# Optimization experiments

Measured on AMD Instinct MI355X. Metric: run time of the kernel, lower is better.

Reference implementation:

```python
import jax, jax.numpy as jnp
from jax import lax
import numpy as np

B, T, L = 8, 24, 145
DHID, DFRAME, DEMB, DGCN, V = 1024, 2500, 128, 512, 1024
PF = 300
DINP = DHID + DFRAME + DEMB + DGCN   # 4164 = LSTM input size
DCONT = DHID + DINP                  # 5188 = cont_t size
FLAT = 64 * 7 * 7                    # 3136
BN_EPS = 1e-5
BN_INV = float(1.0 / np.sqrt(1.0 + BN_EPS))  # eval BN with running mean 0, var 1


def setup_inputs() -> dict:
    key = jax.random.key(0)
    ks = iter(jax.random.split(key, 48))
    rn = lambda *s: jax.random.normal(next(ks), s, jnp.float32)
    w = lambda *s: 0.02 * rn(*s)
    return dict(
        enc=rn(B, L, DHID),
        frames=rn(B, T, 512, 7, 7),
        gcn_embedding=rn(B, DGCN),
        h0=jnp.zeros((B, DHID), jnp.float32),
        c0=jnp.zeros((B, DHID), jnp.float32),
        conv1_w=w(256, 512), conv1_b=jnp.zeros((256,), jnp.float32),
        bn1_g=jnp.ones((256,), jnp.float32), bn1_b=jnp.zeros((256,), jnp.float32),
        conv2_w=w(64, 256), conv2_b=jnp.zeros((64,), jnp.float32),
        bn2_g=jnp.ones((64,), jnp.float32), bn2_b=jnp.zeros((64,), jnp.float32),
        fc_w=w(DFRAME, FLAT), fc_b=jnp.zeros((DFRAME,), jnp.float32),
        hfc_w=w(DHID, DHID), hfc_b=jnp.zeros((DHID,), jnp.float32),
        w_ih=w(4 * DHID, DINP), w_hh=w(4 * DHID, DHID),
        b_ih=jnp.zeros((4 * DHID,), jnp.float32), b_hh=jnp.zeros((4 * DHID,), jnp.float32),
        go=0.1 * rn(DEMB),
        emb_w=w(V, DEMB),
        actor_w=w(DEMB, DCONT), actor_b=jnp.zeros((DEMB,), jnp.float32),
        d1_w=w(FLAT, DCONT), d1_b=jnp.zeros((FLAT,), jnp.float32),
        dconv3_w=w(64, 32, 4, 4), dconv3_b=jnp.zeros((32,), jnp.float32),
        bnm2_g=jnp.ones((32,), jnp.float32), bnm2_b=jnp.zeros((32,), jnp.float32),
        dconv2_w=w(32, 16, 4, 4), dconv2_b=jnp.zeros((16,), jnp.float32),
        bnm1_g=jnp.ones((16,), jnp.float32), bnm1_b=jnp.zeros((16,), jnp.float32),
        dconv1_w=w(16, 1, 4, 4), dconv1_b=jnp.zeros((1,), jnp.float32),
    )


def _bn_eval(x, g, b):
    # BatchNorm2d in eval mode with running_mean=0, running_var=1
    return g[None, :, None, None] * (x * BN_INV) + b[None, :, None, None]


def _up2(x):
    # UpsamplingNearest2d(scale_factor=2)
    return jnp.repeat(jnp.repeat(x, 2, axis=2), 2, axis=3)


def _deconv(x, w, b):
    # ConvTranspose2d(k=4, s=2, p=1); torch weight layout (in, out, kH, kW)
    k = jnp.flip(w, (2, 3)).transpose(1, 0, 2, 3)  # -> (out, in, kH, kW)
    y = lax.conv_general_dilated(x, k, window_strides=(1, 1), padding=((2, 2), (2, 2)),
                                 lhs_dilation=(2, 2),
                                 dimension_numbers=('NCHW', 'OIHW', 'NCHW'))
    return y + b[None, :, None, None]


def reference(enc, frames, gcn_embedding, h0, c0,
              conv1_w, conv1_b, bn1_g, bn1_b, conv2_w, conv2_b, bn2_g, bn2_b, fc_w, fc_b,
              hfc_w, hfc_b, w_ih, w_hh, b_ih, b_hh, go, emb_w, actor_w, actor_b,
              d1_w, d1_b, dconv3_w, dconv3_b, bnm2_g, bnm2_b,
              dconv2_w, dconv2_b, bnm1_g, bnm1_b, dconv1_w, dconv1_b):

    def vis_encode(frame):  # [B,512,7,7] -> [B,DFRAME]
        x = jnp.einsum('bchw,oc->bohw', frame, conv1_w) + conv1_b[None, :, None, None]
        x = jax.nn.relu(_bn_eval(x, bn1_g, bn1_b))
        x = jnp.einsum('bchw,oc->bohw', x, conv2_w) + conv2_b[None, :, None, None]
        x = jax.nn.relu(_bn_eval(x, bn2_g, bn2_b))
        return x.reshape(-1, FLAT) @ fc_w.T + fc_b

    def mask_decode(cont):  # [B,DCONT] -> [B,1,300,300]
        x = jax.nn.relu(cont @ d1_w.T + d1_b).reshape(-1, 64, 7, 7)
        x = _deconv(_up2(x), dconv3_w, dconv3_b)          # 14 -> 28
        x = jax.nn.relu(_bn_eval(x, bnm2_g, bnm2_b))
        x = _deconv(_up2(x), dconv2_w, dconv2_b)          # 56 -> 112
        x = jax.nn.relu(_bn_eval(x, bnm1_g, bnm1_b))
        x = _deconv(x, dconv1_w, dconv1_b)                # 112 -> 224
        return jax.image.resize(x, (x.shape[0], 1, PF, PF), method='bilinear')

    def step(carry, frame_t):
        h, c, e_t = carry
        vis = vis_encode(frame_t)
        hq = h @ hfc_w.T + hfc_b
        score = jax.nn.softmax(jnp.einsum('bld,bd->bl', enc, hq), axis=1)  # [B,L]
        weighted = jnp.einsum('bl,bld->bd', score, enc)
        inp = jnp.concatenate([vis, weighted, e_t, gcn_embedding], axis=1)  # [B,DINP]
        gates = inp @ w_ih.T + b_ih + h @ w_hh.T + b_hh
        i, f, g, o = jnp.split(gates, 4, axis=1)
        c_new = jax.nn.sigmoid(f) * c + jax.nn.sigmoid(i) * jnp.tanh(g)
        h_new = jax.nn.sigmoid(o) * jnp.tanh(c_new)
        cont = jnp.concatenate([h_new, inp], axis=1)  # [B,DCONT]
        action = (cont @ actor_w.T + actor_b) @ emb_w.T  # [B,V]
        mask = mask_decode(cont)
        e_new = emb_w[jnp.argmax(action, axis=1)]  # greedy feed-back
        return (h_new, c_new, e_new), (action, mask, score[:, :, None])

    e0 = jnp.tile(go[None, :], (enc.shape[0], 1))
    (h_T, c_T, _), (actions, masks, attns) = lax.scan(
        step, (h0, c0, e0), jnp.swapaxes(frames, 0, 1))
    out_action = jnp.swapaxes(actions, 0, 1)   # [B,T,V]
    out_mask = jnp.swapaxes(masks, 0, 1)       # [B,T,1,300,300]
    out_attn = jnp.swapaxes(attns, 0, 1)       # [B,T,L,1]
    return (out_action, out_mask, out_attn, h_T, c_T)
```

## Files before the change

### kernel.cpp

```cpp
#include <hip/hip_runtime.h>
#include <cstdint>
#include <cstddef>

#define DEV __device__ __forceinline__
typedef short bf16x8 __attribute__((ext_vector_type(8)));
typedef float fl4 __attribute__((ext_vector_type(4)));
typedef float f32x4 __attribute__((ext_vector_type(4)));
typedef unsigned short u16;

#define BN_INV 0.9999950000375f

DEV float b2f(u16 u){ return __uint_as_float(((unsigned)u)<<16); }
DEV u16 f2b(float f){ unsigned u = __float_as_uint(f); unsigned r = (u + 0x7FFFu + ((u>>16)&1u))>>16; return (u16)r; }

DEV bf16x8 load8(const u16* p){ return *(const bf16x8*)p; }
DEV bf16x8 load8(const float* p){
  fl4 a = *(const fl4*)p; fl4 b = *(const fl4*)(p+4);
  bf16x8 r;
  r[0]=(short)f2b(a[0]); r[1]=(short)f2b(a[1]); r[2]=(short)f2b(a[2]); r[3]=(short)f2b(a[3]);
  r[4]=(short)f2b(b[0]); r[5]=(short)f2b(b[1]); r[6]=(short)f2b(b[2]); r[7]=(short)f2b(b[3]);
  return r;
}


__global__ __launch_bounds__(256) void k_pack_frames(const float* __restrict__ fr, u16* __restrict__ XT){
  int bt = blockIdx.x, tid = threadIdx.x;
  for (int e=0;e<128;e++){
    int flat = e*256 + tid;
    int p = flat>>9, c = flat&511;
    u16 v = 0;
    if (p < 49) v = f2b(fr[((size_t)bt*512 + c)*49 + p]);
    XT[((size_t)bt*64 + p)*512 + c] = v;
  }
}

__global__ __launch_bounds__(256) void k_pack_wseq(const float* __restrict__ w_ih, const float* __restrict__ w_hh,
                                                   u16* __restrict__ wseq){
  int r = blockIdx.x, tid = threadIdx.x;
  const float* wr = w_ih + (size_t)r*4164;
  for (int j=tid;j<2176;j+=256){
    float v = (j < 1024) ? w_hh[(size_t)r*1024 + j] : wr[2500 + (j-1024)];
    wseq[(size_t)r*2176 + j] = f2b(v);
  }
}

__global__ __launch_bounds__(256) void k_pack_dseq(const float* __restrict__ d1_w, const float* __restrict__ actor_w,
                                                   u16* __restrict__ dseq){
  int r = blockIdx.x, tid = threadIdx.x;
  const float* wr = (r < 3136) ? (d1_w + (size_t)r*5188) : (actor_w + (size_t)(r-3136)*5188);
  for (int j=tid;j<2176;j+=256){
    float v = (j < 1024) ? wr[j] : wr[3524 + (j-1024)];
    dseq[(size_t)r*2176 + j] = f2b(v);
  }
}

__global__ __launch_bounds__(256) void k_pack_wvg(const float* __restrict__ w_ih, u16* __restrict__ wvg, int rbase){
  int r = rbase + blockIdx.x, tid = threadIdx.x;
  const float* wr = w_ih + (size_t)r*4164;
  u16* dst = wvg + (size_t)blockIdx.x*3072;
  for (int j=tid;j<3072;j+=256){
    float v = 0.f;
    if (j < 2500) v = wr[j];
    else if (j < 3012) v = wr[3652 + (j-2500)];
    dst[j] = f2b(v);
  }
}

__global__ __launch_bounds__(256) void k_pack_dvg(const float* __restrict__ d1_w, const float* __restrict__ actor_w,
                                                  u16* __restrict__ dvg, int rbase){
  int r = rbase + blockIdx.x, tid = threadIdx.x;
  const float* wr = (r < 3136) ? (d1_w + (size_t)r*5188) : (actor_w + (size_t)(r-3136)*5188);
  u16* dst = dvg + (size_t)blockIdx.x*3072;
  for (int j=tid;j<3072;j+=256){
    float v = 0.f;
    if (j < 2500) v = wr[1024 + j];
    else if (j < 3012) v = wr[4676 + (j-2500)];
    dst[j] = f2b(v);
  }
}

__global__ __launch_bounds__(256) void k_hfcT(const float* __restrict__ hfc_w, u16* __restrict__ hfcT){
  int idx = blockIdx.x*256 + threadIdx.x;
  int k = idx>>10, o = idx&1023;
  hfcT[idx] = f2b(hfc_w[o*1024 + k]);
}

DEV u16 wt_map(const float* w, int n, int k, int CIN, int COUT){
  int o = n % COUT; int cls = n / COUT;
  if (cls >= 4) return 0;
  int py = cls>>1, px = cls&1;
  int i = k/9; int dd = k - i*9; int dy = dd/3, dx = dd - dy*3;
  if (i >= CIN) return 0;
  int ky = (py==0) ? (dy==0 ? 3 : (dy==1 ? 1 : -1)) : (dy==1 ? 2 : (dy==2 ? 0 : -1));
  int kx = (px==0) ? (dx==0 ? 3 : (dx==1 ? 1 : -1)) : (dx==1 ? 2 : (dx==2 ? 0 : -1));
  if (ky < 0 || kx < 0) return 0;
  return f2b(w[((i*COUT + o)*4 + ky)*4 + kx]);
}

__global__ __launch_bounds__(256) void k_misc(
  const float* b_ih, const float* b_hh, const float* d1_b, const float* actor_b,
  const float* emb_w, const float* h0, const float* c0,
  const float* dw3, const float* dw2, const float* dw1,
  float* bias_g, float* bias_da, u16* embT, float* hb0, float* cws,
  u16* Wt3, u16* Wt2, u16* Wt1)
{
  int blk = blockIdx.x, tid = threadIdx.x;
  if (blk < 16){ int i = blk*256+tid; if (i<4096) bias_g[i] = b_ih[i] + b_hh[i]; }
  else if (blk < 29){ int i = (blk-16)*256+tid; if (i<3264) bias_da[i] = (i<3136)? d1_b[i] : actor_b[i-3136]; }
  else if (blk < 541){ int i = (blk-29)*256+tid; int j = i>>10, v = i&1023; embT[i] = f2b(emb_w[v*128 + j]); }
  else if (blk < 573){ int i = (blk-541)*256+tid; if (i<8192){ hb0[i] = h0[i]; cws[i] = c0[i]; } }
  else if (blk < 574){ for (int i=tid;i<2560;i+=256){ int n=i/160, k=i-n*160; Wt1[i] = wt_map(dw1,n,k,16,1); } }
  else if (blk < 590){ for (int i=(blk-574)*256+tid; i<18432; i+=16*256){ int n=i/288, k=i-n*288; Wt2[i] = wt_map(dw2,n,k,32,16); } }
  else { for (int i=(blk-590)*256+tid; i<73728; i+=168*256){ int n=i/576, k=i-n*576; Wt3[i] = wt_map(dw3,n,k,64,32); } }
}

__global__ __launch_bounds__(256) void k_eb(const float* __restrict__ enc, const float* __restrict__ hfc_b, float* __restrict__ eb){
  int li = blockIdx.x*4 + (threadIdx.x>>6);
  int lane = threadIdx.x & 63;
  if (li >= 1160) return;
  const float* ep = enc + (size_t)li*1024;
  float a = 0.f;
  for (int k=lane;k<1024;k+=64) a += ep[k]*hfc_b[k];
  #pragma unroll
  for (int off=32; off; off>>=1) a += __shfl_xor(a, off);
  if (lane == 0) eb[li] = a;
}

__global__ __launch_bounds__(256) void k_vis_in(const u16* __restrict__ Y2, u16* __restrict__ vis_in){
  int bt = blockIdx.x, tid = threadIdx.x;
  for (int f=tid; f<3136; f+=256){
    int c = f/49, p = f - c*49;
    vis_in[(size_t)bt*3136 + f] = Y2[((size_t)bt*64 + p)*64 + c];
  }
}

__global__ __launch_bounds__(256) void k_xin(const u16* __restrict__ vis, const float* __restrict__ gcn, u16* __restrict__ xin2){
  int bt = blockIdx.x, tid = threadIdx.x, b = bt/24;
  for (int j=tid;j<3072;j+=256){
    u16 v = 0;
    if (j < 2500) v = vis[(size_t)bt*2500 + j];
    else if (j < 3012) v = f2b(gcn[b*512 + (j-2500)]);
    xin2[(size_t)bt*3072 + j] = v;
  }
}

template<int OUTB, int ACT, typename TA, typename TB>
__global__ __launch_bounds__(256) void gemm64(
  const TA* __restrict__ A, int lda, const TB* __restrict__ Bm, int ldb,
  void* __restrict__ Cv, int ldc, int M, int N, int K,
  const float* __restrict__ bias, const float* __restrict__ cb, const float* __restrict__ gg, const float* __restrict__ bb)
{
  __shared__ u16 sA[64*72];
  __shared__ u16 sB[64*72];
  int tid = threadIdx.x, lane = tid & 63, w = tid >> 6;
  int wm = w & 1, wn = w >> 1;
  int m0 = blockIdx.x*64, n0 = blockIdx.y*64;
  f32x4 acc[2][2];
  #pragma unroll
  for (int a=0;a<2;a++)
    #pragma unroll
    for (int b=0;b<2;b++){ acc[a][b][0]=0;acc[a][b][1]=0;acc[a][b][2]=0;acc[a][b][3]=0; }

  for (int k0=0;k0<K;k0+=64){
    #pragma unroll
    for (int j=0;j<2;j++){
      int c = tid + 256*j; int row = c>>3; int col = (c&7)*8;
      bf16x8 va = {0,0,0,0,0,0,0,0};
      int gm = m0 + row;
      if (gm < M) va = load8(A + (size_t)gm*lda + k0 + col);
      *(bf16x8*)(&sA[row*72 + col]) = va;
      bf16x8 vb = {0,0,0,0,0,0,0,0};
      int gn = n0 + row;
      if (gn < N) vb = load8(Bm + (size_t)gn*ldb + k0 + col);
      *(bf16x8*)(&sB[row*72 + col]) = vb;
    }
    __syncthreads();
    #pragma unroll
    for (int kk=0;kk<2;kk++){
      bf16x8 af[2], bfv[2];
      #pragma unroll
      for (int tm=0;tm<2;tm++) af[tm]  = *(const bf16x8*)(&sA[(wm*32+tm*16+(lane&15))*72 + kk*32 + (lane>>4)*8]);
      #pragma unroll
      for (int tn=0;tn<2;tn++) bfv[tn] = *(const bf16x8*)(&sB[(wn*32+tn*16+(lane&15))*72 + kk*32 + (lane>>4)*8]);
      #pragma unroll
      for (int tm=0;tm<2;tm++)
        #pragma unroll
        for (int tn=0;tn<2;tn++)
          acc[tm][tn] = __builtin_amdgcn_mfma_f32_16x16x32_bf16(af[tm], bfv[tn], acc[tm][tn], 0,0,0);
    }
    __syncthreads();
  }
  int ml = (lane>>4)*4, nl = lane&15;
  #pragma unroll
  for (int tm=0;tm<2;tm++)
    #pragma unroll
    for (int tn=0;tn<2;tn++)
      #pragma unroll
      for (int r=0;r<4;r++){
        int gm = m0 + wm*32 + tm*16 + ml + r;
        int gn = n0 + wn*32 + tn*16 + nl;
        if (gm < M && gn < N){
          float v = acc[tm][tn][r];
          if (ACT == 0){ if (bias) v += bias[gn]; }
          else { v = (v + cb[gn])*BN_INV*gg[gn] + bb[gn]; v = fmaxf(v, 0.f); }
          if (OUTB) ((u16*)Cv)[(size_t)gm*ldc + gn] = f2b(v);
          else      ((float*)Cv)[(size_t)gm*ldc + gn] = v;
        }
      }
}

template<int OUTB, int NMAJOR, typename TA, typename TB>
__global__ __launch_bounds__(64) void gemm16x(
  const TA* __restrict__ A, int lda, const TB* __restrict__ Bm, int ldb,
  void* __restrict__ Cv, int ldc, int M, int N, int K, const float* __restrict__ bias,
  int MT, int NT)
{
  int nb = gridDim.x;
  int orig = blockIdx.x;
  int q = nb >> 3, r = nb & 7;
  int xcd = orig & 7, j = orig >> 3;
  int wg = (xcd < r ? xcd*(q+1) : r*(q+1) + (xcd-r)*q) + j;
  int bx, by;
  if (NMAJOR){ bx = wg % MT; by = wg / MT; }
  else       { by = wg % NT; bx = wg / NT; }
  int lane = threadIdx.x;
  int m0 = bx*16, n0 = by*16;
  int gm = m0 + (lane&15); if (gm > M-1) gm = M-1;
  int gn = n0 + (lane&15); if (gn > N-1) gn = N-1;
  const TA* ap = A  + (size_t)gm*lda + ((lane>>4)*8);
  const TB* bp = Bm + (size_t)gn*ldb + ((lane>>4)*8);
  f32x4 acc = {0,0,0,0};
  #pragma unroll 4
  for (int ks=0; ks<K; ks+=32){
    bf16x8 a = load8(ap + ks);
    bf16x8 b = load8(bp + ks);
    acc = __builtin_amdgcn_mfma_f32_16x16x32_bf16(a, b, acc, 0,0,0);
  }
  int nn = n0 + (lane&15);
  if (nn >= N) return;
  #pragma unroll
  for (int r2=0;r2<4;r2++){
    int mm = m0 + (lane>>4)*4 + r2;
    if (mm < M){
      float v = acc[r2];
      if (bias) v += bias[nn];
      if (OUTB) ((u16*)Cv)[(size_t)mm*ldc + nn] = f2b(v);
      else      ((float*)Cv)[(size_t)mm*ldc + nn] = v;
    }
  }
}


__global__ __launch_bounds__(256) void p1_scores_action(
  const float* __restrict__ encH, const float* __restrict__ eb,
  const float* __restrict__ hcur, const float* __restrict__ cws,
  float* __restrict__ scores, const float* __restrict__ d1a_out,
  const u16* __restrict__ embT, float* __restrict__ out_act,
  float* __restrict__ cmv, int* __restrict__ cmi,
  float* __restrict__ out_h, float* __restrict__ out_c,
  u16* __restrict__ xb1, int t)
{
  __shared__ float shf[1024];
  __shared__ int shi[256];
  int blk = blockIdx.x, tid = threadIdx.x;
  if (blk < 40){
    if (t == 24) return;
    int b = blk/5, lc = blk - b*5;
    #pragma unroll
    for (int e=0;e<4;e++) shf[tid + 256*e] = hcur[b*1024 + tid + 256*e];
    __syncthreads();
    int w = tid>>6, lane = tid&63;
    for (int i=w;i<29;i+=4){
      int l = lc*29 + i;
      const float* ep = encH + (size_t)(b*145+l)*1024;
      float a = 0.f;
      for (int k=lane;k<1024;k+=64) a += ep[k]*shf[k];
      #pragma unroll
      for (int off=32; off; off>>=1) a += __shfl_xor(a, off);
      if (lane == 0) scores[b*145+l] = a + eb[b*145+l];
    }
  } else if (blk < 72){
    if (t == 0) return;
    int idx = blk-40; int b = idx>>2, vc = idx&3;
    if (tid < 128) shf[tid] = d1a_out[(size_t)(b*24 + t-1)*3264 + 3136 + tid];
    __syncthreads();
    int v = vc*256 + tid;
    float a = 0.f;
    for (int j=0;j<128;j++) a += shf[j]*b2f(embT[j*1024 + v]);
    out_act[(size_t)(b*24 + t-1)*1024 + v] = a;
    shf[256+tid] = a; shi[tid] = v;
    __syncthreads();
    for (int s=128; s; s>>=1){
      if (tid < s){
        float o = shf[256+tid+s]; int oi = shi[tid+s];
        float c = shf[256+tid];   int ci = shi[tid];
        if (o > c || (o == c && oi < ci)){ shf[256+tid] = o; shi[tid] = oi; }
      }
      __syncthreads();
    }
    if (tid == 0){ cmv[b*4+vc] = shf[256]; cmi[b*4+vc] = shi[0]; }
  } else {
    int b = blk-72;
    if (t == 24){
      #pragma unroll
      for (int e=0;e<4;e++){
        int k = tid + 256*e;
        out_h[b*1024+k] = hcur[b*1024+k];
        out_c[b*1024+k] = cws[b*1024+k];
      }
    } else {
      #pragma unroll
      for (int e=0;e<4;e++){
        int k = tid + 256*e;
        xb1[b*2176 + k] = f2b(hcur[b*1024+k]);
      }
    }
  }
}

__global__ __launch_bounds__(256) void p2_softmax_weighted(
  const float* __restrict__ scores, const float* __restrict__ enc,
  float* __restrict__ wgt, float* __restrict__ ecur,
  const float* __restrict__ cmv, const int* __restrict__ cmi,
  const float* __restrict__ emb_w, const float* __restrict__ go,
  float* __restrict__ out_attn, u16* __restrict__ xb1, u16* __restrict__ xb2, int t)
{
  int b = blockIdx.x >> 3, dc = blockIdx.x & 7, tid = threadIdx.x;
  __shared__ float s[145];
  __shared__ float mxs, invs;
  if (tid < 145) s[tid] = scores[b*145+tid];
  __syncthreads();
  if (tid < 64){
    float m = -1e30f;
    for (int i=tid;i<145;i+=64) m = fmaxf(m, s[i]);
    #pragma unroll
    for (int off=32; off; off>>=1) m = fmaxf(m, __shfl_xor(m, off));
    if (tid == 0) mxs = m;
  }
  __syncthreads();
  if (tid < 145) s[tid] = expf(s[tid]-mxs);
  __syncthreads();
  if (tid < 64){
    float sm = 0.f;
    for (int i=tid;i<145;i+=64) sm += s[i];
    #pragma unroll
    for (int off=32; off; off>>=1) sm += __shfl_xor(sm, off);
    if (tid == 0) invs = 1.f/sm;
  }
  __syncthreads();
  float inv = invs;
  if (tid < 128){
    int d = dc*128 + tid;
    float a = 0.f;
    for (int l=0;l<145;l++) a += s[l]*enc[(size_t)(b*145+l)*1024 + d];
    float wv = a*inv;
    wgt[b*1024+d] = wv;
    u16 wb = f2b(wv);
    xb1[b*2176 + 1024 + d] = wb;
    xb2[b*2176 + 1024 + d] = wb;
  } else {
    int i = tid-128;
    if (dc == 0){
      if (i < 145) out_attn[(size_t)(b*24+t)*145 + i] = s[i]*inv;
      int l2 = i + 128;
      if (l2 < 145) out_attn[(size_t)(b*24+t)*145 + l2] = s[l2]*inv;
    } else if (dc == 1){
      float ev;
      if (t == 0) ev = go[i];
      else {
        float bv = cmv[b*4]; int bi = cmi[b*4];
        #pragma unroll
        for (int c=1;c<4;c++){
          float v2 = cmv[b*4+c]; int i2 = cmi[b*4+c];
          if (v2 > bv || (v2 == bv && i2 < bi)){ bv = v2; bi = i2; }
        }
        ev = emb_w[bi*128 + i];
      }
      ecur[b*128+i] = ev;
      u16 eb16 = f2b(ev);
      xb1[b*2176 + 2048 + i] = eb16;
      xb2[b*2176 + 2048 + i] = eb16;
    }
  }
}

__global__ __launch_bounds__(64) void p3m(
  const u16* __restrict__ wseq, const u16* __restrict__ xb, float* __restrict__ gates4)
{
  int lane = threadIdx.x;
  int n = blockIdx.x*16 + (lane & 15);
  const u16* bp = wseq + (size_t)n*2176 + ((lane>>4)*8);
  const u16* ap = xb + (lane&7)*2176 + ((lane>>4)*8);
  f32x4 acc = {0,0,0,0};
  #pragma unroll 4
  for (int kk=0;kk<68;kk++){
    bf16x8 a = *(const bf16x8*)(ap + kk*32);
    bf16x8 b = *(const bf16x8*)(bp + kk*32);
    acc = __builtin_amdgcn_mfma_f32_16x16x32_bf16(a, b, acc, 0,0,0);
  }
  #pragma unroll
  for (int r=0;r<4;r++){
    int m = (lane>>4)*4 + r;
    if (m < 8) gates4[(size_t)m*4096 + n] = acc[r];
  }
}

__global__ __launch_bounds__(256) void p3l(
  const float* __restrict__ gates4, const float* __restrict__ gpre,
  float* __restrict__ hnew, float* __restrict__ cws, u16* __restrict__ xb2, int t)
{
  int idx = blockIdx.x*256 + threadIdx.x;
  int b = idx>>10, J = idx&1023;
  const float* gp = gpre + (size_t)(b*24+t)*4096;
  const float* gb = gates4 + (size_t)b*4096;
  float iv = gb[J]      + gp[J];
  float fv = gb[1024+J] + gp[1024+J];
  float gv = gb[2048+J] + gp[2048+J];
  float ov = gb[3072+J] + gp[3072+J];
  float ig = 1.f/(1.f+expf(-iv));
  float fg = 1.f/(1.f+expf(-fv));
  float gt = tanhf(gv);
  float og = 1.f/(1.f+expf(-ov));
  float cn = fg*cws[idx] + ig*gt;
  cws[idx] = cn;
  float hv = og*tanhf(cn);
  hnew[idx] = hv;
  xb2[b*2176 + J] = f2b(hv);
}

__global__ __launch_bounds__(64) void p4m(
  const u16* __restrict__ dseq, const u16* __restrict__ xb2,
  const float* __restrict__ dpre, float* __restrict__ dout, int t)
{
  int lane = threadIdx.x;
  int R = blockIdx.x*16 + (lane & 15);
  const u16* bp = dseq + (size_t)R*2176 + ((lane>>4)*8);
  const u16* ap = xb2 + (lane&7)*2176 + ((lane>>4)*8);
  f32x4 acc = {0,0,0,0};
  #pragma unroll 4
  for (int kk=0;kk<68;kk++){
    bf16x8 a = *(const bf16x8*)(ap + kk*32);
    bf16x8 b = *(const bf16x8*)(bp + kk*32);
    acc = __builtin_amdgcn_mfma_f32_16x16x32_bf16(a, b, acc, 0,0,0);
  }
  #pragma unroll
  for (int r=0;r<4;r++){
    int m = (lane>>4)*4 + r;
    if (m < 8){
      size_t row = (size_t)(m*24+t)*3264;
      dout[row + R] = acc[r] + dpre[row + R];
    }
  }
}


DEV void stage_tile3(u16* sAt, const float* __restrict__ d1a_bt, int p0, int tid){
  int m = tid & 15;
  int p = p0 + m;
  int u = p / 14, v = p - u*14;
  bool pv = p < 196;
  for (int k = tid>>4; k < 576; k += 16){
    float val = 0.f;
    if (pv){
      int i = k/9; int dd = k - i*9; int dy = dd/3, dx = dd - dy*3;
      int uy = u + dy - 1, vx = v + dx - 1;
      if (uy >= 0 && uy < 14 && vx >= 0 && vx < 14)
        val = fmaxf(d1a_bt[i*49 + (uy>>1)*7 + (vx>>1)], 0.f);
    }
    sAt[m*584 + k] = f2b(val);
  }
}

DEV void stage_tile2(u16* sAt, const float* __restrict__ m1c_bt, int p0, int tid){
  int m = tid & 15;
  int p = p0 + m;
  int u = p / 56, v = p - u*56;
  bool pv = p < 3136;
  for (int k = tid>>4; k < 288; k += 16){
    float val = 0.f;
    if (pv){
      int i = k/9; int dd = k - i*9; int dy = dd/3, dx = dd - dy*3;
      int uy = u + dy - 1, vx = v + dx - 1;
      if (uy >= 0 && uy < 56 && vx >= 0 && vx < 56)
        val = m1c_bt[i*784 + (uy>>1)*28 + (vx>>1)];
    }
    sAt[m*296 + k] = f2b(val);
  }
}

DEV void stage_tile(u16* sAt, int ldk, int Ktot, int Kreal, const float* in_bt, int H, int p0, int tid){
  int m = tid & 15;
  int p = p0 + m;
  int u = p / H, v = p - u*H;
  bool pv = p < H*H;
  for (int k = tid>>4; k < Ktot; k += 16){
    float val = 0.f;
    if (k < Kreal && pv){
      int i = k/9; int dd = k - i*9; int dy = dd/3, dx = dd - dy*3;
      int uy = u + dy - 1, vx = v + dx - 1;
      if (uy >= 0 && uy < H && vx >= 0 && vx < H) val = in_bt[((size_t)i*H + uy)*H + vx];
    }
    sAt[m*ldk + k] = f2b(val);
  }
}

__global__ __launch_bounds__(256) void md3_deconv(const float* __restrict__ d1a_out, int btbase, float* __restrict__ m1c,
  const u16* __restrict__ Wt3, const float* __restrict__ b3, const float* __restrict__ g3, const float* __restrict__ bb3)
{
  __shared__ u16 sAt[16*584];
  int tid = threadIdx.x, lane = tid&63, w = tid>>6;
  int cb = blockIdx.x;
  const float* in_bt = d1a_out + (size_t)(btbase+cb)*3264;
  float* out_bt = m1c + (size_t)cb*32*784;
  int nt = blockIdx.y*4 + w;
  bf16x8 wc[18];
  #pragma unroll
  for (int ks=0;ks<18;ks++) wc[ks] = *(const bf16x8*)(Wt3 + (size_t)(nt*16 + (lane&15))*576 + ks*32 + (lane>>4)*8);
  int cls = nt>>1; int o = (nt&1)*16 + (lane&15);
  int py = cls>>1, px = cls&1;
  float cbv = b3[o], gv = g3[o], bbv = bb3[o];
  int mt = blockIdx.z;
  stage_tile3(sAt, in_bt, mt*16, tid);
  __syncthreads();
  f32x4 acc = {0,0,0,0};
  #pragma unroll
  for (int ks=0;ks<18;ks++){
    bf16x8 a = *(const bf16x8*)(&sAt[(lane&15)*584 + ks*32 + (lane>>4)*8]);
    acc = __builtin_amdgcn_mfma_f32_16x16x32_bf16(a, wc[ks], acc, 0,0,0);
  }
  #pragma unroll
  for (int r=0;r<4;r++){
    int p = mt*16 + (lane>>4)*4 + r;
    if (p < 196){
      int u = p/14, v = p - (p/14)*14;
      float vv = fmaxf((acc[r] + cbv)*BN_INV*gv + bbv, 0.f);
      out_bt[((size_t)o*28 + (2*u+py))*28 + (2*v+px)] = vv;
    }
  }
}

__global__ __launch_bounds__(256) void md2_deconv(const float* __restrict__ m1c, float* __restrict__ m2,
  const u16* __restrict__ Wt2, const float* __restrict__ b2, const float* __restrict__ g2, const float* __restrict__ bb2)
{
  __shared__ u16 sAt[16*296];
  int tid = threadIdx.x, lane = tid&63, w = tid>>6;
  int cb = blockIdx.x;
  const float* in_bt = m1c + (size_t)cb*32*784;
  float* out_bt = m2 + (size_t)cb*16*12544;
  int nt = w;
  bf16x8 wc[9];
  #pragma unroll
  for (int ks=0;ks<9;ks++) wc[ks] = *(const bf16x8*)(Wt2 + (size_t)(nt*16 + (lane&15))*288 + ks*32 + (lane>>4)*8);
  int cls = nt; int o = lane&15;
  int py = cls>>1, px = cls&1;
  float cbv = b2[o], gv = g2[o], bbv = bb2[o];
  int mt = blockIdx.y;
  stage_tile2(sAt, in_bt, mt*16, tid);
  __syncthreads();
  f32x4 acc = {0,0,0,0};
  #pragma unroll
  for (int ks=0;ks<9;ks++){
    bf16x8 a = *(const bf16x8*)(&sAt[(lane&15)*296 + ks*32 + (lane>>4)*8]);
    acc = __builtin_amdgcn_mfma_f32_16x16x32_bf16(a, wc[ks], acc, 0,0,0);
  }
  #pragma unroll
  for (int r=0;r<4;r++){
    int p = mt*16 + (lane>>4)*4 + r;
    if (p < 3136){
      int u = p/56, v = p - u*56;
      float vv = fmaxf((acc[r] + cbv)*BN_INV*gv + bbv, 0.f);
      out_bt[((size_t)o*112 + (2*u+py))*112 + (2*v+px)] = vv;
    }
  }
}

__global__ __launch_bounds__(256) void md1_direct(const float* __restrict__ m2, float* __restrict__ m3,
  const float* __restrict__ dw1, const float* __restrict__ b1)
{
  __shared__ float wl[256];
  int tid = threadIdx.x;
  wl[tid] = dw1[tid];
  __syncthreads();
  int cb = blockIdx.x;
  const float* in_bt = m2 + (size_t)cb*16*12544;
  float* out_bt = m3 + (size_t)cb*50176;
  int idx = blockIdx.y*256 + tid;
  int oy = idx/56, q = idx - oy*56;
  int ox0 = q*4;
  int iyA = (oy+1)>>1;  bool vA = iyA < 112;
  int iyB = iyA - 1;    bool vB = iyB >= 0;
  int kyA = (oy&1) ? 0 : 1;
  int kyB = kyA + 2;
  int xb = (ox0>>1) - 1;
  bool v0 = xb >= 0, v3 = (xb+3) < 112;
  int x0 = v0 ? xb : 0, x3 = v3 ? xb+3 : 111;
  float mA = vA ? 1.f : 0.f, mB = vB ? 1.f : 0.f;
  float mA0 = v0 ? mA : 0.f, mA3 = v3 ? mA : 0.f;
  float mB0 = v0 ? mB : 0.f, mB3 = v3 ? mB : 0.f;
  const float* rA = in_bt + (size_t)(vA ? iyA : 0)*112;
  const float* rB = in_bt + (size_t)(vB ? iyB : 0)*112;
  float acc0=0.f, acc1=0.f, acc2=0.f, acc3=0.f;
  #pragma unroll 4
  for (int i=0;i<16;i++){
    const float* cA = rA + i*12544;
    const float* cB = rB + i*12544;
    float a0 = cA[x0]*mA0, a1 = cA[xb+1]*mA, a2 = cA[xb+2]*mA, a3 = cA[x3]*mA3;
    float b0 = cB[x0]*mB0, b1v = cB[xb+1]*mB, b2 = cB[xb+2]*mB, b3 = cB[x3]*mB3;
    fl4 wA = *(const fl4*)(&wl[i*16 + kyA*4]);
    fl4 wB = *(const fl4*)(&wl[i*16 + kyB*4]);
    acc0 += a1*wA[1] + a0*wA[3] + b1v*wB[1] + b0*wB[3];
    acc1 += a2*wA[0] + a1*wA[2] + b2*wB[0] + b1v*wB[2];
    acc2 += a2*wA[1] + a1*wA[3] + b2*wB[1] + b1v*wB[3];
    acc3 += a3*wA[0] + a2*wA[2] + b3*wB[0] + b2*wB[2];
  }
  float bv = b1[0];
  fl4 o4 = {acc0+bv, acc1+bv, acc2+bv, acc3+bv};
  *(fl4*)(out_bt + (size_t)oy*224 + ox0) = o4;
}

__global__ __launch_bounds__(256) void k_resize(const float* __restrict__ m3, float* __restrict__ out_mask, int btbase){
  int cb = blockIdx.x;
  const float* in_bt = m3 + (size_t)cb*50176;
  int idx = blockIdx.y*256 + threadIdx.x;
  if (idx >= 90000) return;
  int oy = idx/300, ox = idx - oy*300;
  const float sc = 224.f/300.f;
  float sy = (oy+0.5f)*sc - 0.5f;
  float sx = (ox+0.5f)*sc - 0.5f;
  float fy = floorf(sy), fx = floorf(sx);
  float wy = sy-fy, wx = sx-fx;
  int y0 = (int)fy, x0 = (int)fx;
  int y0c = min(max(y0,0),223), y1c = min(max(y0+1,0),223);
  int x0c = min(max(x0,0),223), x1c = min(max(x0+1,0),223);
  float v00 = in_bt[y0c*224+x0c], v01 = in_bt[y0c*224+x1c];
  float v10 = in_bt[y1c*224+x0c], v11 = in_bt[y1c*224+x1c];
  float v = (1.f-wy)*((1.f-wx)*v00 + wx*v01) + wy*((1.f-wx)*v10 + wx*v11);
  out_mask[(size_t)(btbase+cb)*90000 + idx] = v;
}


extern "C" void kernel_launch(void* const* d_in, const int* in_sizes, int n_in,
                              void* d_out, int out_size, void* d_ws, size_t ws_size,
                              hipStream_t stream)
{
  const float* enc      = (const float*)d_in[0];
  const float* frames   = (const float*)d_in[1];
  const float* gcn      = (const float*)d_in[2];
  const float* h0       = (const float*)d_in[3];
  const float* c0       = (const float*)d_in[4];
  const float* conv1_w  = (const float*)d_in[5];
  const float* conv1_b  = (const float*)d_in[6];
  const float* bn1_g    = (const float*)d_in[7];
  const float* bn1_b    = (const float*)d_in[8];
  const float* conv2_w  = (const float*)d_in[9];
  const float* conv2_b  = (const float*)d_in[10];
  const float* bn2_g    = (const float*)d_in[11];
  const float* bn2_b    = (const float*)d_in[12];
  const float* fc_w     = (const float*)d_in[13];
  const float* fc_b     = (const float*)d_in[14];
  const float* hfc_w    = (const float*)d_in[15];
  const float* hfc_b    = (const float*)d_in[16];
  const float* w_ih     = (const float*)d_in[17];
  const float* w_hh     = (const float*)d_in[18];
  const float* b_ih     = (const float*)d_in[19];
  const float* b_hh     = (const float*)d_in[20];
  const float* go       = (const float*)d_in[21];
  const float* emb_w    = (const float*)d_in[22];
  const float* actor_w  = (const float*)d_in[23];
  const float* actor_b  = (const float*)d_in[24];
  const float* d1_w     = (const float*)d_in[25];
  const float* d1_b     = (const float*)d_in[26];
  const float* dconv3_w = (const float*)d_in[27];
  const float* dconv3_b = (const float*)d_in[28];
  const float* bnm2_g   = (const float*)d_in[29];
  const float* bnm2_b   = (const float*)d_in[30];
  const float* dconv2_w = (const float*)d_in[31];
  const float* dconv2_b = (const float*)d_in[32];
  const float* bnm1_g   = (const float*)d_in[33];
  const float* bnm1_b   = (const float*)d_in[34];
  const float* dconv1_w = (const float*)d_in[35];
  const float* dconv1_b = (const float*)d_in[36];
  (void)in_sizes; (void)n_in; (void)out_size;

  float* obase    = (float*)d_out;
  float* out_act  = obase;
  float* out_mask = obase + 196608;
  float* out_attn = obase + 17476608;
  float* out_h    = obase + 17504448;
  float* out_c    = obase + 17512640;

  char* ob = (char*)out_mask;
  size_t ooff = 0;
  auto oalloc = [&](size_t bytes)->char*{ char* p = ob + ooff; ooff = (ooff + bytes + 255) & ~(size_t)255; return p; };
  u16*   wseq      = (u16*)  oalloc(4096ULL*2176*2);
  u16*   dseq      = (u16*)  oalloc(3264ULL*2176*2);
  float* encH      = (float*)oalloc(1160ULL*1024*4);
  float* gates_pre = (float*)oalloc(192ULL*4096*4);
  float* d1a_pre   = (float*)oalloc(192ULL*3264*4);
  u16*   xin2      = (u16*)  oalloc(192ULL*3072*2);
  u16*   XT     = (u16*)oalloc(12288ULL*512*2);
  u16*   Y1     = (u16*)oalloc(12288ULL*256*2);
  u16*   Y2     = (u16*)oalloc(12288ULL*64*2);
  u16*   vis_in = (u16*)oalloc(192ULL*3136*2);
  u16*   vis    = (u16*)oalloc(192ULL*2500*2);
  u16*   wchunk = XT;

  char* wsb = (char*)d_ws;
  size_t off = 0;
  auto alloc = [&](size_t bytes)->char*{ char* p = wsb + off; off = (off + bytes + 255) & ~(size_t)255; return p; };
  float* d1a_out   = (float*)alloc(192ULL*3264*4);
  u16*   embT      = (u16*)  alloc(128ULL*1024*2);
  float* eb        = (float*)alloc(1160ULL*4);
  u16*   Wt3       = (u16*)  alloc(128ULL*576*2);
  u16*   Wt2       = (u16*)  alloc(64ULL*288*2);
  u16*   Wt1       = (u16*)  alloc(16ULL*160*2);
  float* hb        = (float*)alloc(2ULL*8192*4);
  float* c_ws      = (float*)alloc(8192ULL*4);
  float* e_cur     = (float*)alloc(8ULL*128*4);
  float* weighted  = (float*)alloc(8192ULL*4);
  float* scores_raw= (float*)alloc(8ULL*145*4);
  float* cmv       = (float*)alloc(32ULL*4);
  int*   cmi       = (int*)  alloc(32ULL*4);
  float* bias_g    = (float*)alloc(4096ULL*4);
  float* bias_da   = (float*)alloc(3264ULL*4);
  u16*   xb1       = (u16*)  alloc(8ULL*2176*2);
  u16*   xb2       = (u16*)  alloc(8ULL*2176*2);
  float* gates4    = (float*)alloc(8ULL*4096*4);
  size_t zbase = off;
  u16*   hfcT = (u16*)alloc(1024ULL*1024*2);

  const int cands[10] = {48,24,16,12,8,6,4,3,2,1};
  int C = 1;
  for (int i=0;i<10;i++){
    size_t need = zbase + (size_t)cands[i]*1103872ULL + 65536;
    if (need <= ws_size){ C = cands[i]; break; }
  }
  size_t mo = zbase;
  auto malloc_ = [&](size_t bytes)->char*{ char* p = wsb + mo; mo = (mo + bytes + 255) & ~(size_t)255; return p; };
  float* m1c  = (float*)malloc_((size_t)C*32*784*4);
  float* m2b  = (float*)malloc_((size_t)C*16*12544*4);
  float* m3b  = (float*)malloc_((size_t)C*50176*4);

  k_pack_frames<<<192, 256, 0, stream>>>(frames, XT);
  k_pack_wseq<<<4096, 256, 0, stream>>>(w_ih, w_hh, wseq);
  k_pack_dseq<<<3264, 256, 0, stream>>>(d1_w, actor_w, dseq);
  k_hfcT<<<4096, 256, 0, stream>>>(hfc_w, hfcT);
  k_misc<<<758, 256, 0, stream>>>(b_ih, b_hh, d1_b, actor_b, emb_w, h0, c0,
                                  dconv3_w, dconv2_w, dconv1_w,
                                  bias_g, bias_da, embT, hb, c_ws, Wt3, Wt2, Wt1);
  k_eb<<<290, 256, 0, stream>>>(enc, hfc_b, eb);

  gemm64<1,1><<<dim3(192,4), 256, 0, stream>>>(XT, 512, conv1_w, 512, Y1, 256, 12288, 256, 512, nullptr, conv1_b, bn1_g, bn1_b);
  gemm64<1,1><<<dim3(192,1), 256, 0, stream>>>(Y1, 256, conv2_w, 256, Y2, 64, 12288, 64, 256, nullptr, conv2_b, bn2_g, bn2_b);
  k_vis_in<<<192, 256, 0, stream>>>(Y2, vis_in);
  gemm16x<1,1><<<12*157, 64, 0, stream>>>(vis_in, 3136, fc_w, 3136, vis, 2500, 192, 2500, 3136, fc_b, 12, 157);
  k_xin<<<192, 256, 0, stream>>>(vis, gcn, xin2);
  gemm16x<0,0><<<73*64, 64, 0, stream>>>(enc, 1024, hfcT, 1024, encH, 1024, 1160, 1024, 1024, nullptr, 73, 64);

  for (int c=0;c<2;c++){
    k_pack_wvg<<<2048, 256, 0, stream>>>(w_ih, wchunk, c*2048);
    gemm16x<0,1><<<12*128, 64, 0, stream>>>(xin2, 3072, wchunk, 3072, gates_pre + c*2048, 4096,
                                            192, 2048, 3072, bias_g + c*2048, 12, 128);
  }
  for (int c=0;c<2;c++){
    k_pack_dvg<<<1632, 256, 0, stream>>>(d1_w, actor_w, wchunk, c*1632);
    gemm16x<0,1><<<12*102, 64, 0, stream>>>(xin2, 3072, wchunk, 3072, d1a_pre + c*1632, 3264,
                                            192, 1632, 3072, bias_da + c*1632, 12, 102);
  }

  for (int t=0; t<=24; t++){
    float* hcur = hb + (t&1)*8192;
    float* hnew = hb + ((t+1)&1)*8192;
    p1_scores_action<<<80, 256, 0, stream>>>(encH, eb, hcur, c_ws, scores_raw, d1a_out, embT,
                                             out_act, cmv, cmi, out_h, out_c, xb1, t);
    if (t == 24) break;
    p2_softmax_weighted<<<64, 256, 0, stream>>>(scores_raw, enc, weighted, e_cur, cmv, cmi, emb_w, go,
                                                out_attn, xb1, xb2, t);
    p3m<<<256, 64, 0, stream>>>(wseq, xb1, gates4);
    p3l<<<32, 256, 0, stream>>>(gates4, gates_pre, hnew, c_ws, xb2, t);
    p4m<<<204, 64, 0, stream>>>(dseq, xb2, d1a_pre, d1a_out, t);
  }

  for (int btbase=0; btbase<192; btbase+=C){
    md3_deconv<<<dim3(C,2,13), 256, 0, stream>>>(d1a_out, btbase, m1c, Wt3, dconv3_b, bnm2_g, bnm2_b);
    md2_deconv<<<dim3(C,196), 256, 0, stream>>>(m1c, m2b, Wt2, dconv2_b, bnm1_g, bnm1_b);
    md1_direct<<<dim3(C,49), 256, 0, stream>>>(m2b, m3b, dconv1_w, dconv1_b);
    k_resize<<<dim3(C,352), 256, 0, stream>>>(m3b, out_mask, btbase);
  }
}
```

Baseline: 3.137 ms.

## Pre-pack fc weights to bf16, remap blocks across XCDs, deepen GEMV unroll

Adds a pre-pass that converts the fc weight matrix to bf16 before the visual fc GEMM, so the GEMM no longer converts fp32 to bf16 inside its inner loop. It remaps block indices in the per-step kernels (p1, p2, p3m, d1 GEMV) so that consecutive rows land on the same XCD for L2 locality. It also raises loop unrolling from 4 to 8 in the MFMA GEMV loops and deletes an unused helper. The extra pack pass reads and writes the fc weight matrix once more, and the higher unroll may raise register use.

```diff
diff --git a/kernel.cpp b/kernel.cpp
--- a/kernel.cpp
+++ b/kernel.cpp
@@ -52,6 +52,13 @@
     float v = (j < 1024) ? wr[j] : wr[3524 + (j-1024)];
     dseq[(size_t)r*2176 + j] = f2b(v);
   }
+}
+
+__global__ __launch_bounds__(256) void k_pack_fcw(const float* __restrict__ fc_w, u16* __restrict__ fcwB){
+  int r = blockIdx.x, tid = threadIdx.x;
+  const float* wr = fc_w + (size_t)r*3136;
+  u16* dst = fcwB + (size_t)r*3136;
+  for (int j=tid;j<3136;j+=256) dst[j] = f2b(wr[j]);
 }
 
 __global__ __launch_bounds__(256) void k_pack_wvg(const float* __restrict__ w_ih, u16* __restrict__ wvg, int rbase){
@@ -230,7 +237,7 @@
   const TA* ap = A  + (size_t)gm*lda + ((lane>>4)*8);
   const TB* bp = Bm + (size_t)gn*ldb + ((lane>>4)*8);
   f32x4 acc = {0,0,0,0};
-  #pragma unroll 4
+  #pragma unroll 8
   for (int ks=0; ks<K; ks+=32){
     bf16x8 a = load8(ap + ks);
     bf16x8 b = load8(bp + ks);
@@ -265,7 +272,7 @@
   int blk = blockIdx.x, tid = threadIdx.x;
   if (blk < 40){
     if (t == 24) return;
-    int b = blk/5, lc = blk - b*5;
+    int b = blk & 7, lc = blk >> 3;
     #pragma unroll
     for (int e=0;e<4;e++) shf[tid + 256*e] = hcur[b*1024 + tid + 256*e];
     __syncthreads();
@@ -325,7 +332,7 @@
   const float* __restrict__ emb_w, const float* __restrict__ go,
   float* __restrict__ out_attn, u16* __restrict__ xb1, u16* __restrict__ xb2, int t)
 {
-  int b = blockIdx.x >> 3, dc = blockIdx.x & 7, tid = threadIdx.x;
+  int b = blockIdx.x & 7, dc = blockIdx.x >> 3, tid = threadIdx.x;
   __shared__ float s[145];
   __shared__ float mxs, invs;
   if (tid < 145) s[tid] = scores[b*145+tid];
@@ -387,12 +394,14 @@
 __global__ __launch_bounds__(64) void p3m(
   const u16* __restrict__ wseq, const u16* __restrict__ xb, float* __restrict__ gates4)
 {
+  int orig = blockIdx.x;
+  int blk = (orig & 7)*32 + (orig >> 3);
   int lane = threadIdx.x;
-  int n = blockIdx.x*16 + (lane & 15);
+  int n = blk*16 + (lane & 15);
   const u16* bp = wseq + (size_t)n*2176 + ((lane>>4)*8);
   const u16* ap = xb + (lane&7)*2176 + ((lane>>4)*8);
   f32x4 acc = {0,0,0,0};
-  #pragma unroll 4
+  #pragma unroll 8
   for (int kk=0;kk<68;kk++){
     bf16x8 a = *(const bf16x8*)(ap + kk*32);
     bf16x8 b = *(const bf16x8*)(bp + kk*32);
@@ -432,12 +441,15 @@
   const u16* __restrict__ dseq, const u16* __restrict__ xb2,
   const float* __restrict__ dpre, float* __restrict__ dout, int t)
 {
+  int orig = blockIdx.x;
+  int xcd = orig & 7, j = orig >> 3;
+  int blk = (xcd < 4 ? xcd*26 : 104 + (xcd-4)*25) + j;
   int lane = threadIdx.x;
-  int R = blockIdx.x*16 + (lane & 15);
+  int R = blk*16 + (lane & 15);
   const u16* bp = dseq + (size_t)R*2176 + ((lane>>4)*8);
   const u16* ap = xb2 + (lane&7)*2176 + ((lane>>4)*8);
   f32x4 acc = {0,0,0,0};
-  #pragma unroll 4
+  #pragma unroll 8
   for (int kk=0;kk<68;kk++){
     bf16x8 a = *(const bf16x8*)(ap + kk*32);
     bf16x8 b = *(const bf16x8*)(bp + kk*32);
@@ -485,22 +497,6 @@
         val = m1c_bt[i*784 + (uy>>1)*28 + (vx>>1)];
     }
     sAt[m*296 + k] = f2b(val);
-  }
-}
-
-DEV void stage_tile(u16* sAt, int ldk, int Ktot, int Kreal, const float* in_bt, int H, int p0, int tid){
-  int m = tid & 15;
-  int p = p0 + m;
-  int u = p / H, v = p - u*H;
-  bool pv = p < H*H;
-  for (int k = tid>>4; k < Ktot; k += 16){
-    float val = 0.f;
-    if (k < Kreal && pv){
-      int i = k/9; int dd = k - i*9; int dy = dd/3, dx = dd - dy*3;
-      int uy = u + dy - 1, vx = v + dx - 1;
-      if (uy >= 0 && uy < H && vx >= 0 && vx < H) val = in_bt[((size_t)i*H + uy)*H + vx];
-    }
-    sAt[m*ldk + k] = f2b(val);
   }
 }
 
@@ -704,6 +700,7 @@
   u16*   vis_in = (u16*)oalloc(192ULL*3136*2);
   u16*   vis    = (u16*)oalloc(192ULL*2500*2);
   u16*   wchunk = XT;
+  u16*   fcwB   = XT;
 
   char* wsb = (char*)d_ws;
   size_t off = 0;
@@ -753,7 +750,8 @@
   gemm64<1,1><<<dim3(192,4), 256, 0, stream>>>(XT, 512, conv1_w, 512, Y1, 256, 12288, 256, 512, nullptr, conv1_b, bn1_g, bn1_b);
   gemm64<1,1><<<dim3(192,1), 256, 0, stream>>>(Y1, 256, conv2_w, 256, Y2, 64, 12288, 64, 256, nullptr, conv2_b, bn2_g, bn2_b);
   k_vis_in<<<192, 256, 0, stream>>>(Y2, vis_in);
-  gemm16x<1,1><<<12*157, 64, 0, stream>>>(vis_in, 3136, fc_w, 3136, vis, 2500, 192, 2500, 3136, fc_b, 12, 157);
+  k_pack_fcw<<<2500, 256, 0, stream>>>(fc_w, fcwB);
+  gemm16x<1,1><<<12*157, 64, 0, stream>>>(vis_in, 3136, fcwB, 3136, vis, 2500, 192, 2500, 3136, fc_b, 12, 157);
   k_xin<<<192, 256, 0, stream>>>(vis, gcn, xin2);
   gemm16x<0,0><<<73*64, 64, 0, stream>>>(enc, 1024, hfcT, 1024, encH, 1024, 1160, 1024, 1024, nullptr, 73, 64);
 
```

Measured after the change: 2.925 ms. -6.8%, faster.
